# Performance work log

Measured on AMD Instinct MI355X. Metric: run time of the kernel, lower is better.

Reference implementation:

```python
import jax, jax.numpy as jnp
import numpy as np

N = 20000
E = 320000
HEADS = 4
CH = [128, 256, 256]


def setup_inputs() -> dict:
    key = jax.random.key(0)
    ks = jax.random.split(key, 16)
    x = jax.random.normal(ks[0], (N, CH[0]), dtype=jnp.float32)
    edge_index = jax.random.randint(ks[1], (2, E), 0, N, dtype=jnp.int64)

    def glorot(k, shape, fan_in):
        return jax.random.normal(k, shape, dtype=jnp.float32) / np.float32(np.sqrt(fan_in))

    # Block 0: FeaStConv 128 -> 256, skip Linear 128 -> 256
    W0 = glorot(ks[2], (CH[0], HEADS * CH[1]), CH[0])
    u0 = glorot(ks[3], (CH[0], HEADS), CH[0])
    c0 = jnp.zeros((HEADS,), jnp.float32)
    b0 = jnp.zeros((CH[1],), jnp.float32)
    skipW0 = glorot(ks[4], (CH[0], CH[1]), CH[0])
    skipb0 = jnp.zeros((CH[1],), jnp.float32)
    # Block 1: FeaStConv 256 -> 256, identity skip
    W1 = glorot(ks[5], (CH[1], HEADS * CH[2]), CH[1])
    u1 = glorot(ks[6], (CH[1], HEADS), CH[1])
    c1 = jnp.zeros((HEADS,), jnp.float32)
    b1 = jnp.zeros((CH[2],), jnp.float32)
    return {"x": x, "edge_index": edge_index,
            "W0": W0, "u0": u0, "c0": c0, "b0": b0,
            "skipW0": skipW0, "skipb0": skipb0,
            "W1": W1, "u1": u1, "c1": c1, "b1": b1}


def feast_conv(x, src, dst, W, u, c, b):
    """FeaStConv: out_i = b + mean_{j in N(i)} sum_h softmax_h(u_h.(x_j-x_i)+c_h) * W_h x_j."""
    n = x.shape[0]
    out_ch = W.shape[1] // HEADS
    y = (x @ W).reshape(n, HEADS, out_ch)              # [N, H, out]
    q = jax.nn.softmax((x[src] - x[dst]) @ u + c, -1)  # [E', H]
    msg = jnp.einsum('eh,ehd->ed', q, y[src])          # [E', out]
    s = jax.ops.segment_sum(msg, dst, num_segments=n)
    cnt = jax.ops.segment_sum(jnp.ones(src.shape, x.dtype), dst, num_segments=n)
    return s / jnp.maximum(cnt, 1.0)[:, None] + b


def reference(x, edge_index, W0, u0, c0, b0, skipW0, skipb0, W1, u1, c1, b1):
    n = x.shape[0]
    loop = jnp.arange(n, dtype=edge_index.dtype)       # self-loops (PyG default)
    src = jnp.concatenate([edge_index[0], loop])
    dst = jnp.concatenate([edge_index[1], loop])
    # ResBlock 0: relu(conv(x) + linear skip) -- channels change 128->256
    h = jax.nn.relu(feast_conv(x, src, dst, W0, u0, c0, b0) + x @ skipW0 + skipb0)
    # ResBlock 1: relu(conv(h) + identity skip)
    h = jax.nn.relu(feast_conv(h, src, dst, W1, u1, c1, b1) + h)
    return (h, edge_index)
```

## Files before the change

kernel.cpp:

```cpp
#include <hip/hip_runtime.h>
#include <hip/hip_bf16.h>

typedef __hip_bfloat16 bf16;

typedef short bf16x8 __attribute__((ext_vector_type(8)));
typedef float f32x4  __attribute__((ext_vector_type(4)));

__device__ __forceinline__ float bflo(unsigned v){ union{unsigned u; float f;} c; c.u = v << 16; return c.f; }
__device__ __forceinline__ float bfhi(unsigned v){ union{unsigned u; float f;} c; c.u = v & 0xffff0000u; return c.f; }
__device__ __forceinline__ unsigned cvtpk_bf16(float lo, float hi){
  unsigned r;
  asm("v_cvt_pk_bf16_f32 %0, %1, %2" : "=v"(r) : "v"(lo), "v"(hi));
  return r;
}

__device__ __forceinline__ void dev_t32(
    const bf16* __restrict__ B, int ldB, int sr, int sc,
    bf16* __restrict__ Bt, int ldBt, int dr, int dc,
    int t, bf16 (*tile)[33])
{
  const int tx = t & 31, ty = t >> 5;
  #pragma unroll
  for (int i = 0; i < 32; i += 8)
    tile[ty + i][tx] = B[(size_t)(sr + ty + i) * ldB + sc + tx];
  __syncthreads();
  #pragma unroll
  for (int i = 0; i < 32; i += 8)
    Bt[(size_t)(dr + ty + i) * ldBt + dc + tx] = tile[tx][ty + i];
}

__global__ __launch_bounds__(256) void prep_kernel(
    const bf16* __restrict__ x, const int* __restrict__ ei,
    const bf16* __restrict__ W0, const bf16* __restrict__ sW0,
    const bf16* __restrict__ W1, const bf16* __restrict__ u0,
    bf16* __restrict__ Btc0, bf16* __restrict__ Bt1,
    int* __restrict__ deg, float* __restrict__ eout, float4* __restrict__ p0,
    int N, int E, int b4, int b5)
{
  __shared__ bf16 tile[32][33];
  const int bid = blockIdx.x;
  const int t   = threadIdx.x;

  if (bid < 128) {
    const int bx = bid & 31, by = bid >> 5;
    dev_t32(W0, 1024, by * 32, bx * 32,
            Btc0, 640, (bx & 7) * 32, (bx >> 3) * 128 + by * 32, t, tile);
  } else if (bid < 160) {
    const int lb = bid - 128, bx = lb & 7, by = lb >> 3;
    dev_t32(sW0, 256, by * 32, bx * 32,
            Btc0, 640, bx * 32, 512 + by * 32, t, tile);
  } else if (bid < 416) {
    const int lb = bid - 160, bx = lb & 31, by = lb >> 5;
    dev_t32(W1, 1024, by * 32, bx * 32,
            Bt1, 1024, (bx & 7) * 32, (bx >> 3) * 256 + by * 32, t, tile);
  } else if (bid < b4) {
    const int e = (bid - 416) * 256 + t;
    if (e < E) atomicAdd(deg + ei[E + e], 1);
  } else if (bid < b5) {
    const int i = (bid - b4) * 256 + t;
    if (i < 2 * E) eout[i] = (float)ei[i];
  } else {
    const int node = (bid - b5) * 4 + (t >> 6);
    if (node >= N) return;
    const int lane = t & 63;
    const unsigned xv = ((const unsigned*)(x + (size_t)node * 128))[lane];
    const float d0 = bflo(xv), d1 = bfhi(xv);
    const uint4 uv = *(const uint4*)(u0 + (size_t)lane * 8);
    float t0 = d0 * bflo(uv.x) + d1 * bflo(uv.z);
    float t1 = d0 * bfhi(uv.x) + d1 * bfhi(uv.z);
    float t2 = d0 * bflo(uv.y) + d1 * bflo(uv.w);
    float t3 = d0 * bfhi(uv.y) + d1 * bfhi(uv.w);
    #pragma unroll
    for (int off = 32; off > 0; off >>= 1) {
      t0 += __shfl_xor(t0, off);
      t1 += __shfl_xor(t1, off);
      t2 += __shfl_xor(t2, off);
      t3 += __shfl_xor(t3, off);
    }
    if (lane == 0) p0[node] = make_float4(t0, t1, t2, t3);
  }
}

template<int MODE>
__global__ __launch_bounds__(256) void gemm_cat_kernel(
    const bf16* __restrict__ A1, int K1, const bf16* __restrict__ A2, int K2,
    const bf16* __restrict__ Bt, int ldBt, int M,
    const bf16* __restrict__ bias1, const bf16* __restrict__ bias2,
    const bf16* __restrict__ hadd, bf16* __restrict__ outb,
    float* __restrict__ outf)
{
  __shared__ __align__(16) bf16 As[64 * 64];
  __shared__ __align__(16) bf16 Bs[64 * 64];

  const int tid  = threadIdx.x;
  const int col0 = blockIdx.x * 64;
  const int row0 = blockIdx.y * 64;
  const int lane = tid & 63;
  const int wave = tid >> 6;
  const int wm   = wave & 1, wn = wave >> 1;
  const int ln   = lane & 15, quad = lane >> 4;
  const int K    = K1 + K2;

  f32x4 acc[2][2] = {};

  for (int k0 = 0; k0 < K; k0 += 64) {
    #pragma unroll
    for (int rep = 0; rep < 2; ++rep) {
      const int c  = tid + rep * 256;
      const int r  = c >> 3;
      const int kp = (c & 7) << 3;
      const int gr = min(row0 + r, M - 1);
      const int kk = k0 + kp;
      uint4 va;
      if (kk < K1) va = *(const uint4*)(A1 + (size_t)gr * K1 + kk);
      else         va = *(const uint4*)(A2 + (size_t)gr * K2 + (kk - K1));
      *(uint4*)(As + r * 64 + (kp ^ ((r & 7) << 3))) = va;
    }
    #pragma unroll
    for (int rep = 0; rep < 2; ++rep) {
      const int c  = tid + rep * 256;
      const int r  = c >> 3;
      const int kp = (c & 7) << 3;
      *(uint4*)(Bs + r * 64 + (kp ^ ((r & 7) << 3))) =
          *(const uint4*)(Bt + (size_t)(col0 + r) * ldBt + k0 + kp);
    }
    __syncthreads();

    bf16x8 a[2][2], b[2][2];
    #pragma unroll
    for (int mi = 0; mi < 2; ++mi) {
      const int rr = wm * 32 + mi * 16 + ln;
      #pragma unroll
      for (int ks = 0; ks < 2; ++ks)
        a[mi][ks] = *(const bf16x8*)(As + rr * 64 + ((ks * 32 + quad * 8) ^ ((rr & 7) << 3)));
    }
    #pragma unroll
    for (int ni = 0; ni < 2; ++ni) {
      const int rr = wn * 32 + ni * 16 + ln;
      #pragma unroll
      for (int ks = 0; ks < 2; ++ks)
        b[ni][ks] = *(const bf16x8*)(Bs + rr * 64 + ((ks * 32 + quad * 8) ^ ((rr & 7) << 3)));
    }
    #pragma unroll
    for (int ks = 0; ks < 2; ++ks)
      #pragma unroll
      for (int mi = 0; mi < 2; ++mi)
        #pragma unroll
        for (int ni = 0; ni < 2; ++ni)
          acc[mi][ni] = __builtin_amdgcn_mfma_f32_16x16x32_bf16(a[mi][ks], b[ni][ks], acc[mi][ni], 0, 0, 0);
    __syncthreads();
  }

  #pragma unroll
  for (int mi = 0; mi < 2; ++mi) {
    const int rbase = row0 + wm * 32 + mi * 16 + quad * 4;
    #pragma unroll
    for (int ni = 0; ni < 2; ++ni) {
      const int col = col0 + wn * 32 + ni * 16 + ln;
      float bb = __bfloat162float(bias1[col]);
      if (MODE == 0) bb += __bfloat162float(bias2[col]);
      #pragma unroll
      for (int r = 0; r < 4; ++r) {
        const int gr = rbase + r;
        if (gr >= M) continue;
        const size_t idx = (size_t)gr * 256 + col;
        float v = acc[mi][ni][r] + bb;
        if (MODE == 1) v += __bfloat162float(hadd[idx]);
        v = fmaxf(v, 0.f);
        if (MODE == 0) outb[idx] = __float2bfloat16(v);
        else           outf[idx] = v;
      }
    }
  }
}

__global__ __launch_bounds__(256) void scan_kernel(
    const int* __restrict__ deg, int* __restrict__ rowptr, int N)
{
  __shared__ int part[256];
  const int t = threadIdx.x;
  const int chunk = (N + 255) / 256;
  const int start = t * chunk;
  const int stop  = min(start + chunk, N);
  int sum = 0;
  for (int j = start; j < stop; ++j) sum += deg[j];
  part[t] = sum;
  __syncthreads();
  for (int off = 1; off < 256; off <<= 1) {
    int v = (t >= off) ? part[t - off] : 0;
    __syncthreads();
    part[t] += v;
    __syncthreads();
  }
  int base = (t == 0) ? 0 : part[t - 1];
  for (int j = start; j < stop; ++j) { rowptr[j] = base; base += deg[j]; }
  if (t == 255) rowptr[N] = part[255];
}

__global__ __launch_bounds__(256) void scatter_kernel(
    const int* __restrict__ ei, const int* __restrict__ rowptr,
    int* __restrict__ cursor, int* __restrict__ ssrc, int E)
{
  const int e = (int)((unsigned)blockIdx.x * 256u + threadIdx.x);
  if (e >= E) return;
  const int src = ei[e];
  const int d   = ei[E + e];
  const int pp  = rowptr[d] + atomicAdd(cursor + d, 1);
  ssrc[pp] = src;
}

__global__ __launch_bounds__(256) void proj256_kernel(
    const bf16* __restrict__ h, const bf16* __restrict__ u,
    float4* __restrict__ p, int N)
{
  const int node = (int)(((unsigned)blockIdx.x * 256u + threadIdx.x) >> 6);
  if (node >= N) return;
  const int lane = threadIdx.x & 63;
  const uint2 hv = *(const uint2*)(h + (size_t)node * 256 + lane * 4);
  const float d0 = bflo(hv.x), d1 = bfhi(hv.x);
  const float d2 = bflo(hv.y), d3 = bfhi(hv.y);
  const uint4 ua = *(const uint4*)(u + (size_t)lane * 16);
  const uint4 ub = *(const uint4*)(u + (size_t)lane * 16 + 8);
  float t0 = d0*bflo(ua.x) + d1*bflo(ua.z) + d2*bflo(ub.x) + d3*bflo(ub.z);
  float t1 = d0*bfhi(ua.x) + d1*bfhi(ua.z) + d2*bfhi(ub.x) + d3*bfhi(ub.z);
  float t2 = d0*bflo(ua.y) + d1*bflo(ua.w) + d2*bflo(ub.y) + d3*bflo(ub.w);
  float t3 = d0*bfhi(ua.y) + d1*bfhi(ua.w) + d2*bfhi(ub.y) + d3*bfhi(ub.w);
  #pragma unroll
  for (int off = 32; off > 0; off >>= 1) {
    t0 += __shfl_xor(t0, off);
    t1 += __shfl_xor(t1, off);
    t2 += __shfl_xor(t2, off);
    t3 += __shfl_xor(t3, off);
  }
  if (lane == 0) p[node] = make_float4(t0, t1, t2, t3);
}

template<int CIN>
__global__ __launch_bounds__(256) void passF_kernel(
    const int* __restrict__ rowptr, const int* __restrict__ ssrc,
    const float4* __restrict__ p, const bf16* __restrict__ feat,
    const bf16* __restrict__ cvec, bf16* __restrict__ F, int N)
{
  __shared__ int    s_src[4][64];
  __shared__ float4 s_q[4][64];

  const int t = threadIdx.x;
  const int g = t >> 6;
  const int l = t & 63;
  const int i = blockIdx.x * 4 + g;
  if (i >= N) return;

  const int h2 = l >> 5;
  const int c  = l & 31;
  const int beg = rowptr[i];
  const int deg = rowptr[i + 1] - beg;

  constexpr int CPL = (CIN == 128) ? 4 : 8;
  constexpr int SH  = (CIN == 128) ? 8 : 9;
  const unsigned coff = (unsigned)c * (CPL * 2);
  const char* fb = (const char*)feat;

  const float cc0 = __bfloat162float(cvec[0]), cc1 = __bfloat162float(cvec[1]);
  const float cc2 = __bfloat162float(cvec[2]), cc3 = __bfloat162float(cvec[3]);
  const float4 pd = p[i];

  float f[4][CPL];
  #pragma unroll
  for (int h = 0; h < 4; ++h)
    #pragma unroll
    for (int k = 0; k < CPL; ++k) f[h][k] = 0.f;

#define PF_ACC(OFF, QX, QY, QZ, QW)                                            \
  if constexpr (CIN == 128) {                                                  \
    const uint2 v_ = *(const uint2*)(fb + (OFF));                              \
    const float d0 = bflo(v_.x), d1 = bfhi(v_.x);                              \
    const float d2 = bflo(v_.y), d3 = bfhi(v_.y);                              \
    f[0][0] += (QX)*d0; f[0][1] += (QX)*d1; f[0][2] += (QX)*d2; f[0][3] += (QX)*d3; \
    f[1][0] += (QY)*d0; f[1][1] += (QY)*d1; f[1][2] += (QY)*d2; f[1][3] += (QY)*d3; \
    f[2][0] += (QZ)*d0; f[2][1] += (QZ)*d1; f[2][2] += (QZ)*d2; f[2][3] += (QZ)*d3; \
    f[3][0] += (QW)*d0; f[3][1] += (QW)*d1; f[3][2] += (QW)*d2; f[3][3] += (QW)*d3; \
  } else {                                                                     \
    const uint4 v_ = *(const uint4*)(fb + (OFF));                              \
    const float d0 = bflo(v_.x), d1 = bfhi(v_.x);                              \
    const float d2 = bflo(v_.y), d3 = bfhi(v_.y);                              \
    const float d4 = bflo(v_.z), d5 = bfhi(v_.z);                              \
    const float d6 = bflo(v_.w), d7 = bfhi(v_.w);                              \
    f[0][0] += (QX)*d0; f[0][1] += (QX)*d1; f[0][2] += (QX)*d2; f[0][3] += (QX)*d3; \
    f[0][4] += (QX)*d4; f[0][5] += (QX)*d5; f[0][6] += (QX)*d6; f[0][7] += (QX)*d7; \
    f[1][0] += (QY)*d0; f[1][1] += (QY)*d1; f[1][2] += (QY)*d2; f[1][3] += (QY)*d3; \
    f[1][4] += (QY)*d4; f[1][5] += (QY)*d5; f[1][6] += (QY)*d6; f[1][7] += (QY)*d7; \
    f[2][0] += (QZ)*d0; f[2][1] += (QZ)*d1; f[2][2] += (QZ)*d2; f[2][3] += (QZ)*d3; \
    f[2][4] += (QZ)*d4; f[2][5] += (QZ)*d5; f[2][6] += (QZ)*d6; f[2][7] += (QZ)*d7; \
    f[3][0] += (QW)*d0; f[3][1] += (QW)*d1; f[3][2] += (QW)*d2; f[3][3] += (QW)*d3; \
    f[3][4] += (QW)*d4; f[3][5] += (QW)*d5; f[3][6] += (QW)*d6; f[3][7] += (QW)*d7; \
  }

  {
    const float mx = fmaxf(fmaxf(cc0, cc1), fmaxf(cc2, cc3));
    const float e0 = __expf(cc0 - mx), e1 = __expf(cc1 - mx);
    const float e2 = __expf(cc2 - mx), e3 = __expf(cc3 - mx);
    const float sinv = 1.f / (e0 + e1 + e2 + e3);
    if (h2 == 0) {
      const unsigned off = ((unsigned)i << SH) + coff;
      PF_ACC(off, e0 * sinv, e1 * sinv, e2 * sinv, e3 * sinv)
    }
  }

#define PF_PAIR(P)                                                             \
  {                                                                            \
    const int e_ = ((P) << 1) + h2;                                            \
    const int    src_ = s_src[g][e_];                                          \
    const float4 q_   = s_q[g][e_];                                            \
    const unsigned off_ = ((unsigned)src_ << SH) + coff;                       \
    PF_ACC(off_, q_.x, q_.y, q_.z, q_.w)                                       \
  }

  for (int c0 = 0; c0 < deg; c0 += 64) {
    const int cnt = min(64, deg - c0);
    if (l < cnt) {
      const int s = ssrc[beg + c0 + l];
      const float4 ps = p[s];
      const float t0 = ps.x - pd.x + cc0;
      const float t1 = ps.y - pd.y + cc1;
      const float t2 = ps.z - pd.z + cc2;
      const float t3 = ps.w - pd.w + cc3;
      const float mx = fmaxf(fmaxf(t0, t1), fmaxf(t2, t3));
      const float e0 = __expf(t0 - mx), e1 = __expf(t1 - mx);
      const float e2 = __expf(t2 - mx), e3 = __expf(t3 - mx);
      const float inv = 1.f / (e0 + e1 + e2 + e3);
      s_src[g][l] = s;
      s_q[g][l]   = make_float4(e0 * inv, e1 * inv, e2 * inv, e3 * inv);
    } else if (l == cnt) {
      s_src[g][l] = 0;
      s_q[g][l]   = make_float4(0.f, 0.f, 0.f, 0.f);
    }
    const int np = (cnt + 1) >> 1;
    int pj = 0;
    for (; pj + 8 <= np; pj += 8) {
      PF_PAIR(pj)     PF_PAIR(pj + 1) PF_PAIR(pj + 2) PF_PAIR(pj + 3)
      PF_PAIR(pj + 4) PF_PAIR(pj + 5) PF_PAIR(pj + 6) PF_PAIR(pj + 7)
    }
    for (; pj + 4 <= np; pj += 4) { PF_PAIR(pj) PF_PAIR(pj + 1) PF_PAIR(pj + 2) PF_PAIR(pj + 3) }
    for (; pj < np; ++pj) PF_PAIR(pj)
  }
#undef PF_PAIR
#undef PF_ACC

  const float s = 1.f / (float)(deg + 1);
  #pragma unroll
  for (int h = 0; h < 4; ++h)
    #pragma unroll
    for (int k = 0; k < CPL; ++k) {
      float v = f[h][k] * s;
      v += __shfl_xor(v, 32);
      f[h][k] = v;
    }

  if constexpr (CIN == 128) {
    char* dst = (char*)F + ((size_t)i << 10) + (unsigned)c * 8;
    if (h2 == 0) {
      uint2 p0v, p1v;
      p0v.x = cvtpk_bf16(f[0][0], f[0][1]); p0v.y = cvtpk_bf16(f[0][2], f[0][3]);
      p1v.x = cvtpk_bf16(f[1][0], f[1][1]); p1v.y = cvtpk_bf16(f[1][2], f[1][3]);
      *(uint2*)(dst)       = p0v;
      *(uint2*)(dst + 256) = p1v;
    } else {
      uint2 p2v, p3v;
      p2v.x = cvtpk_bf16(f[2][0], f[2][1]); p2v.y = cvtpk_bf16(f[2][2], f[2][3]);
      p3v.x = cvtpk_bf16(f[3][0], f[3][1]); p3v.y = cvtpk_bf16(f[3][2], f[3][3]);
      *(uint2*)(dst + 512) = p2v;
      *(uint2*)(dst + 768) = p3v;
    }
  } else {
    char* dst = (char*)F + ((size_t)i << 11) + (unsigned)c * 16;
    if (h2 == 0) {
      uint4 p0v, p1v;
      p0v.x = cvtpk_bf16(f[0][0], f[0][1]); p0v.y = cvtpk_bf16(f[0][2], f[0][3]);
      p0v.z = cvtpk_bf16(f[0][4], f[0][5]); p0v.w = cvtpk_bf16(f[0][6], f[0][7]);
      p1v.x = cvtpk_bf16(f[1][0], f[1][1]); p1v.y = cvtpk_bf16(f[1][2], f[1][3]);
      p1v.z = cvtpk_bf16(f[1][4], f[1][5]); p1v.w = cvtpk_bf16(f[1][6], f[1][7]);
      *(uint4*)(dst)        = p0v;
      *(uint4*)(dst + 512)  = p1v;
    } else {
      uint4 p2v, p3v;
      p2v.x = cvtpk_bf16(f[2][0], f[2][1]); p2v.y = cvtpk_bf16(f[2][2], f[2][3]);
      p2v.z = cvtpk_bf16(f[2][4], f[2][5]); p2v.w = cvtpk_bf16(f[2][6], f[2][7]);
      p3v.x = cvtpk_bf16(f[3][0], f[3][1]); p3v.y = cvtpk_bf16(f[3][2], f[3][3]);
      p3v.z = cvtpk_bf16(f[3][4], f[3][5]); p3v.w = cvtpk_bf16(f[3][6], f[3][7]);
      *(uint4*)(dst + 1024) = p2v;
      *(uint4*)(dst + 1536) = p3v;
    }
  }
}

extern "C" void kernel_launch(void* const* d_in, const int* in_sizes, int n_in,
                              void* d_out, int out_size, void* d_ws, size_t ws_size,
                              hipStream_t stream)
{
  const bf16* x   = (const bf16*)d_in[0];
  const int*  ei  = (const int*)d_in[1];
  const bf16* W0  = (const bf16*)d_in[2];
  const bf16* u0  = (const bf16*)d_in[3];
  const bf16* c0  = (const bf16*)d_in[4];
  const bf16* b0  = (const bf16*)d_in[5];
  const bf16* sW0 = (const bf16*)d_in[6];
  const bf16* sb0 = (const bf16*)d_in[7];
  const bf16* W1  = (const bf16*)d_in[8];
  const bf16* u1  = (const bf16*)d_in[9];
  const bf16* c1  = (const bf16*)d_in[10];
  const bf16* b1  = (const bf16*)d_in[11];

  const int N = in_sizes[0] / 128;
  const int E = in_sizes[1] / 2;

  char* ws = (char*)d_ws;
  bf16*   F      = (bf16*)ws;   ws += (size_t)N * 1024 * sizeof(bf16);
  bf16*   h0     = (bf16*)ws;   ws += (size_t)N * 256 * sizeof(bf16);
  float4* p0     = (float4*)ws; ws += (size_t)N * sizeof(float4);
  float4* p1     = (float4*)ws; ws += (size_t)N * sizeof(float4);
  int*    ssrc   = (int*)ws;    ws += (size_t)E * sizeof(int);
  int*    deg    = (int*)ws;    ws += (size_t)N * sizeof(int);
  int*    cursor = (int*)ws;    ws += (size_t)N * sizeof(int);
  int*    rowptr = (int*)ws;    ws += ((size_t)N + 1) * sizeof(int);
  bf16*   Btc0   = (bf16*)ws;   ws += (size_t)256 * 640 * sizeof(bf16);
  bf16*   Bt1    = (bf16*)ws;   ws += (size_t)256 * 1024 * sizeof(bf16);

  hipMemsetAsync(deg, 0, 2 * (size_t)N * sizeof(int), stream);

  const int eBlocks  = (E + 255) / 256;
  const int gTiles   = (N + 63) / 64;
  const int nwBlocks = (N + 3) / 4;

  const int b4 = 416 + eBlocks;
  const int b5 = b4 + (2 * E + 255) / 256;
  const int b6 = b5 + nwBlocks;

  prep_kernel<<<b6, 256, 0, stream>>>(x, ei, W0, sW0, W1, u0, Btc0, Bt1,
                                      deg, (float*)d_out + (size_t)N * 256, p0,
                                      N, E, b4, b5);
  scan_kernel<<<1, 256, 0, stream>>>(deg, rowptr, N);
  scatter_kernel<<<eBlocks, 256, 0, stream>>>(ei, rowptr, cursor, ssrc, E);

  passF_kernel<128><<<nwBlocks, 256, 0, stream>>>(rowptr, ssrc, p0, x, c0, F, N);
  gemm_cat_kernel<0><<<dim3(4, gTiles), 256, 0, stream>>>(
      F, 512, x, 128, Btc0, 640, N, b0, sb0, nullptr, h0, nullptr);

  proj256_kernel<<<nwBlocks, 256, 0, stream>>>(h0, u1, p1, N);
  passF_kernel<256><<<nwBlocks, 256, 0, stream>>>(rowptr, ssrc, p1, h0, c1, F, N);
  gemm_cat_kernel<1><<<dim3(4, gTiles), 256, 0, stream>>>(
      F, 1024, nullptr, 0, Bt1, 1024, N, b1, nullptr, h0, nullptr, (float*)d_out);
}
```

Before: 269.7 us.

## Fuse layer-1 aggregation with its GEMM via shared-memory tile; merge degree count into edge copy

Layer 1 no longer writes the N×1024 aggregated feature matrix to global memory and reads it back in a separate GEMM. Each 512-thread block now builds a 32-row tile of it in swizzled LDS (64 KB) and multiplies it against the transposed W1 with MFMA, applying bias, residual and ReLU in the epilogue. Separately, the prep kernel folds the degree atomics into the edge-index-to-float copy, which removes one group of blocks. The tradeoffs are a large LDS footprint per block that limits occupancy, B operands streamed from global memory without reuse across blocks, and a GEMM that now waits behind the irregular gather.

```diff
diff --git a/kernel.cpp b/kernel.cpp
--- a/kernel.cpp
+++ b/kernel.cpp
@@ -35,7 +35,7 @@
     const bf16* __restrict__ W1, const bf16* __restrict__ u0,
     bf16* __restrict__ Btc0, bf16* __restrict__ Bt1,
     int* __restrict__ deg, float* __restrict__ eout, float4* __restrict__ p0,
-    int N, int E, int b4, int b5)
+    int N, int E, int b5)
 {
   __shared__ bf16 tile[32][33];
   const int bid = blockIdx.x;
@@ -53,12 +53,13 @@
     const int lb = bid - 160, bx = lb & 31, by = lb >> 5;
     dev_t32(W1, 1024, by * 32, bx * 32,
             Bt1, 1024, (bx & 7) * 32, (bx >> 3) * 256 + by * 32, t, tile);
-  } else if (bid < b4) {
-    const int e = (bid - 416) * 256 + t;
-    if (e < E) atomicAdd(deg + ei[E + e], 1);
   } else if (bid < b5) {
-    const int i = (bid - b4) * 256 + t;
-    if (i < 2 * E) eout[i] = (float)ei[i];
+    const int i = (bid - 416) * 256 + t;
+    if (i < 2 * E) {
+      const int v = ei[i];
+      eout[i] = (float)v;
+      if (i >= E) atomicAdd(deg + v, 1);
+    }
   } else {
     const int node = (bid - b5) * 4 + (t >> 6);
     if (node >= N) return;
@@ -393,6 +394,173 @@
   }
 }
 
+__global__ __launch_bounds__(512) void fusedF_gemm_kernel(
+    const int* __restrict__ rowptr, const int* __restrict__ ssrc,
+    const float4* __restrict__ p, const bf16* __restrict__ h0,
+    const bf16* __restrict__ cvec, const bf16* __restrict__ Bt,
+    const bf16* __restrict__ bias, float* __restrict__ outf, int N)
+{
+  __shared__ __align__(16) bf16 Fs[32 * 1024];
+  __shared__ int    s_src[8][64];
+  __shared__ float4 s_q[8][64];
+
+  const int t  = threadIdx.x;
+  const int w  = t >> 6;
+  const int l  = t & 63;
+  const int i0 = blockIdx.x * 32;
+
+  const int h2 = l >> 5;
+  const int c  = l & 31;
+  const unsigned coff = (unsigned)c * 16;
+  const char* fb = (const char*)h0;
+
+  const float cc0 = __bfloat162float(cvec[0]), cc1 = __bfloat162float(cvec[1]);
+  const float cc2 = __bfloat162float(cvec[2]), cc3 = __bfloat162float(cvec[3]);
+  float sl0, sl1, sl2, sl3;
+  {
+    const float mx = fmaxf(fmaxf(cc0, cc1), fmaxf(cc2, cc3));
+    const float e0 = __expf(cc0 - mx), e1 = __expf(cc1 - mx);
+    const float e2 = __expf(cc2 - mx), e3 = __expf(cc3 - mx);
+    const float sinv = 1.f / (e0 + e1 + e2 + e3);
+    sl0 = e0 * sinv; sl1 = e1 * sinv; sl2 = e2 * sinv; sl3 = e3 * sinv;
+  }
+
+#define FG_ACC(OFF, QX, QY, QZ, QW)                                            \
+  {                                                                            \
+    const uint4 v_ = *(const uint4*)(fb + (OFF));                              \
+    const float d0 = bflo(v_.x), d1 = bfhi(v_.x);                              \
+    const float d2 = bflo(v_.y), d3 = bfhi(v_.y);                              \
+    const float d4 = bflo(v_.z), d5 = bfhi(v_.z);                              \
+    const float d6 = bflo(v_.w), d7 = bfhi(v_.w);                              \
+    f[0][0] += (QX)*d0; f[0][1] += (QX)*d1; f[0][2] += (QX)*d2; f[0][3] += (QX)*d3; \
+    f[0][4] += (QX)*d4; f[0][5] += (QX)*d5; f[0][6] += (QX)*d6; f[0][7] += (QX)*d7; \
+    f[1][0] += (QY)*d0; f[1][1] += (QY)*d1; f[1][2] += (QY)*d2; f[1][3] += (QY)*d3; \
+    f[1][4] += (QY)*d4; f[1][5] += (QY)*d5; f[1][6] += (QY)*d6; f[1][7] += (QY)*d7; \
+    f[2][0] += (QZ)*d0; f[2][1] += (QZ)*d1; f[2][2] += (QZ)*d2; f[2][3] += (QZ)*d3; \
+    f[2][4] += (QZ)*d4; f[2][5] += (QZ)*d5; f[2][6] += (QZ)*d6; f[2][7] += (QZ)*d7; \
+    f[3][0] += (QW)*d0; f[3][1] += (QW)*d1; f[3][2] += (QW)*d2; f[3][3] += (QW)*d3; \
+    f[3][4] += (QW)*d4; f[3][5] += (QW)*d5; f[3][6] += (QW)*d6; f[3][7] += (QW)*d7; \
+  }
+#define FG_PAIR(P)                                                             \
+  {                                                                            \
+    const int e_ = ((P) << 1) + h2;                                            \
+    const int    src_ = s_src[w][e_];                                          \
+    const float4 q_   = s_q[w][e_];                                            \
+    FG_ACC(((size_t)src_ << 9) + coff, q_.x, q_.y, q_.z, q_.w)                 \
+  }
+
+  for (int nn = 0; nn < 4; ++nn) {
+    const int r = (w << 2) + nn;
+    const int i = i0 + r;
+    if (i < N) {
+      const int beg = rowptr[i];
+      const int deg = rowptr[i + 1] - beg;
+      const float4 pd = p[i];
+
+      float f[4][8];
+      #pragma unroll
+      for (int h = 0; h < 4; ++h)
+        #pragma unroll
+        for (int k = 0; k < 8; ++k) f[h][k] = 0.f;
+
+      if (h2 == 0) FG_ACC(((size_t)i << 9) + coff, sl0, sl1, sl2, sl3)
+
+      for (int c0 = 0; c0 < deg; c0 += 64) {
+        const int cnt = min(64, deg - c0);
+        if (l < cnt) {
+          const int s = ssrc[beg + c0 + l];
+          const float4 ps = p[s];
+          const float t0 = ps.x - pd.x + cc0;
+          const float t1 = ps.y - pd.y + cc1;
+          const float t2 = ps.z - pd.z + cc2;
+          const float t3 = ps.w - pd.w + cc3;
+          const float mx = fmaxf(fmaxf(t0, t1), fmaxf(t2, t3));
+          const float e0 = __expf(t0 - mx), e1 = __expf(t1 - mx);
+          const float e2 = __expf(t2 - mx), e3 = __expf(t3 - mx);
+          const float inv = 1.f / (e0 + e1 + e2 + e3);
+          s_src[w][l] = s;
+          s_q[w][l]   = make_float4(e0 * inv, e1 * inv, e2 * inv, e3 * inv);
+        } else if (l == cnt) {
+          s_src[w][l] = 0;
+          s_q[w][l]   = make_float4(0.f, 0.f, 0.f, 0.f);
+        }
+        const int np = (cnt + 1) >> 1;
+        int pj = 0;
+        for (; pj + 8 <= np; pj += 8) {
+          FG_PAIR(pj)     FG_PAIR(pj + 1) FG_PAIR(pj + 2) FG_PAIR(pj + 3)
+          FG_PAIR(pj + 4) FG_PAIR(pj + 5) FG_PAIR(pj + 6) FG_PAIR(pj + 7)
+        }
+        for (; pj + 4 <= np; pj += 4) { FG_PAIR(pj) FG_PAIR(pj + 1) FG_PAIR(pj + 2) FG_PAIR(pj + 3) }
+        for (; pj < np; ++pj) FG_PAIR(pj)
+      }
+
+      const float sc = 1.f / (float)(deg + 1);
+      #pragma unroll
+      for (int h = 0; h < 4; ++h)
+        #pragma unroll
+        for (int k = 0; k < 8; ++k) {
+          float v = f[h][k] * sc;
+          v += __shfl_xor(v, 32);
+          f[h][k] = v;
+        }
+      const int hb = h2 * 2;
+      uint4 pka, pkb;
+      pka.x = cvtpk_bf16(f[hb][0], f[hb][1]);   pka.y = cvtpk_bf16(f[hb][2], f[hb][3]);
+      pka.z = cvtpk_bf16(f[hb][4], f[hb][5]);   pka.w = cvtpk_bf16(f[hb][6], f[hb][7]);
+      pkb.x = cvtpk_bf16(f[hb+1][0], f[hb+1][1]); pkb.y = cvtpk_bf16(f[hb+1][2], f[hb+1][3]);
+      pkb.z = cvtpk_bf16(f[hb+1][4], f[hb+1][5]); pkb.w = cvtpk_bf16(f[hb+1][6], f[hb+1][7]);
+      const int swz = (r & 7) << 3;
+      *(uint4*)(Fs + r * 1024 + (((hb    ) * 256 + c * 8) ^ swz)) = pka;
+      *(uint4*)(Fs + r * 1024 + (((hb + 1) * 256 + c * 8) ^ swz)) = pkb;
+    }
+  }
+#undef FG_PAIR
+#undef FG_ACC
+
+  __syncthreads();
+
+  const int ln = l & 15, quad = l >> 4;
+  const int colb = w * 32;
+  f32x4 acc[2][2] = {};
+
+  #pragma unroll 2
+  for (int k0 = 0; k0 < 1024; k0 += 32) {
+    bf16x8 a[2], b[2];
+    #pragma unroll
+    for (int mi = 0; mi < 2; ++mi) {
+      const int rr = mi * 16 + ln;
+      a[mi] = *(const bf16x8*)(Fs + rr * 1024 + ((k0 + quad * 8) ^ ((rr & 7) << 3)));
+    }
+    #pragma unroll
+    for (int ni = 0; ni < 2; ++ni) {
+      const int col = colb + ni * 16 + ln;
+      b[ni] = *(const bf16x8*)(Bt + (size_t)col * 1024 + k0 + quad * 8);
+    }
+    #pragma unroll
+    for (int mi = 0; mi < 2; ++mi)
+      #pragma unroll
+      for (int ni = 0; ni < 2; ++ni)
+        acc[mi][ni] = __builtin_amdgcn_mfma_f32_16x16x32_bf16(a[mi], b[ni], acc[mi][ni], 0, 0, 0);
+  }
+
+  #pragma unroll
+  for (int mi = 0; mi < 2; ++mi) {
+    #pragma unroll
+    for (int ni = 0; ni < 2; ++ni) {
+      const int col = colb + ni * 16 + ln;
+      const float bb = __bfloat162float(bias[col]);
+      #pragma unroll
+      for (int rj = 0; rj < 4; ++rj) {
+        const int node = i0 + mi * 16 + quad * 4 + rj;
+        if (node >= N) continue;
+        const size_t idx = (size_t)node * 256 + col;
+        const float v = acc[mi][ni][rj] + bb + __bfloat162float(h0[idx]);
+        outf[idx] = fmaxf(v, 0.f);
+      }
+    }
+  }
+}
+
 extern "C" void kernel_launch(void* const* d_in, const int* in_sizes, int n_in,
                               void* d_out, int out_size, void* d_ws, size_t ws_size,
                               hipStream_t stream)
@@ -414,7 +582,7 @@
   const int E = in_sizes[1] / 2;
 
   char* ws = (char*)d_ws;
-  bf16*   F      = (bf16*)ws;   ws += (size_t)N * 1024 * sizeof(bf16);
+  bf16*   F      = (bf16*)ws;   ws += (size_t)N * 512 * sizeof(bf16);
   bf16*   h0     = (bf16*)ws;   ws += (size_t)N * 256 * sizeof(bf16);
   float4* p0     = (float4*)ws; ws += (size_t)N * sizeof(float4);
   float4* p1     = (float4*)ws; ws += (size_t)N * sizeof(float4);
@@ -430,14 +598,14 @@
   const int eBlocks  = (E + 255) / 256;
   const int gTiles   = (N + 63) / 64;
   const int nwBlocks = (N + 3) / 4;
-
-  const int b4 = 416 + eBlocks;
-  const int b5 = b4 + (2 * E + 255) / 256;
+  const int fgBlocks = (N + 31) / 32;
+
+  const int b5 = 416 + (2 * E + 255) / 256;
   const int b6 = b5 + nwBlocks;
 
   prep_kernel<<<b6, 256, 0, stream>>>(x, ei, W0, sW0, W1, u0, Btc0, Bt1,
                                       deg, (float*)d_out + (size_t)N * 256, p0,
-                                      N, E, b4, b5);
+                                      N, E, b5);
   scan_kernel<<<1, 256, 0, stream>>>(deg, rowptr, N);
   scatter_kernel<<<eBlocks, 256, 0, stream>>>(ei, rowptr, cursor, ssrc, E);
 
@@ -446,7 +614,6 @@
       F, 512, x, 128, Btc0, 640, N, b0, sb0, nullptr, h0, nullptr);
 
   proj256_kernel<<<nwBlocks, 256, 0, stream>>>(h0, u1, p1, N);
-  passF_kernel<256><<<nwBlocks, 256, 0, stream>>>(rowptr, ssrc, p1, h0, c1, F, N);
-  gemm_cat_kernel<1><<<dim3(4, gTiles), 256, 0, stream>>>(
-      F, 1024, nullptr, 0, Bt1, 1024, N, b1, nullptr, h0, nullptr, (float*)d_out);
-}
+  fusedF_gemm_kernel<<<fgBlocks, 512, 0, stream>>>(rowptr, ssrc, p1, h0, c1,
+                                                   Bt1, b1, (float*)d_out, N);
+}
```

Result: slower. 343.2 us (+27.3%).
